# Performance work log

Measured on AMD Instinct MI355X. Metric: run time of the kernel, lower is better.

The kernel has to match this reference:

```python
import jax, jax.numpy as jnp
import numpy as np

N, E, IN_DIM, D, T, L, B, SLEN, C = 50000, 600000, 128, 128, 4, 2, 2048, 16, 16


def _deg_inv_sqrt(idx, n, dtype):
    deg = jax.ops.segment_sum(jnp.ones(idx.shape, dtype=dtype), idx, num_segments=n)
    return jnp.where(deg > 0, deg ** -0.5, 0.0).astype(dtype)


def gcn_conv(h, edge_index, W, b):
    # PyG GCNConv: add self loops, symmetric norm, x@W, scatter-add, +bias
    n = h.shape[0]
    loop = jnp.arange(n)
    row = jnp.concatenate([edge_index[0], loop])
    col = jnp.concatenate([edge_index[1], loop])
    dis = _deg_inv_sqrt(col, n, h.dtype)
    norm = dis[row] * dis[col]              # [E+N]
    xw = h @ W                               # [N, D]
    msgs = xw[row] * norm[:, None]           # [E+N, D] gather
    out = jax.ops.segment_sum(msgs, col, num_segments=n)
    return out + b


def re_conv(r, edge_index, node_type, W, wtype, b):
    # REConv(norm='both'): left-norm by src out-degree, x@W, type weight,
    # scatter-add to dst, right-norm by dst in-degree, +bias, relu
    n = r.shape[0]
    row, col = edge_index
    dl = _deg_inv_sqrt(row, n, r.dtype)
    x = (r * dl[:, None]) @ W                # [N, T]
    x = x * wtype[node_type][:, None]
    out = jax.ops.segment_sum(x[row], col, num_segments=n)
    dr = _deg_inv_sqrt(col, n, r.dtype)
    out = out * dr[:, None] + b
    return jax.nn.relu(out)


def setup_inputs() -> dict:
    key = jax.random.key(0)
    ks = jax.random.split(key, 10)
    x = jax.random.normal(ks[0], (N, IN_DIM), dtype=jnp.float32)
    label = jax.random.randint(ks[1], (N,), 0, C)
    seqs = jax.random.randint(ks[2], (B, SLEN), 0, N)
    edge_index = jax.random.randint(ks[3], (2, E), 0, N)
    node_type = jnp.sort(jax.random.randint(ks[4], (N,), 0, T))
    s_in = 1.0 / np.sqrt(IN_DIM)
    s_d = 1.0 / np.sqrt(D)
    fcW = jax.random.normal(ks[5], (T, IN_DIM, D), dtype=jnp.float32) * s_in
    fcB = jnp.zeros((T, D), dtype=jnp.float32)
    gcnW = jax.random.normal(ks[6], (L, D, D), dtype=jnp.float32) * s_d
    gcnB = jnp.zeros((L, D), dtype=jnp.float32)
    reW = jax.random.normal(ks[7], (L, T, T), dtype=jnp.float32) * 0.5
    re_wtype = jnp.ones((L, T), dtype=jnp.float32)
    reB = jnp.zeros((L, T), dtype=jnp.float32)
    predW = jax.random.normal(ks[8], (D, C), dtype=jnp.float32) * s_d
    predB = jnp.zeros((C,), dtype=jnp.float32)
    return {"x": x, "label": label, "seqs": seqs, "edge_index": edge_index,
            "node_type": node_type, "fcW": fcW, "fcB": fcB, "gcnW": gcnW,
            "gcnB": gcnB, "reW": reW, "re_wtype": re_wtype, "reB": reB,
            "predW": predW, "predB": predB}


def reference(x, label, seqs, edge_index, node_type, fcW, fcB, gcnW, gcnB,
              reW, re_wtype, reB, predW, predB):
    n = x.shape[0]
    # per-type input projection; node_type is sorted so this equals
    # torch.cat([fc[t](x[node_type==t]) for t])
    h_all = jnp.einsum('ni,tio->tno', x, fcW) + fcB[:, None, :]  # [T, N, D]
    gh = h_all[node_type, jnp.arange(n)]                          # [N, D]
    r = jnp.eye(fcW.shape[0], dtype=x.dtype)[node_type]           # [N, T]
    for l in range(gcnW.shape[0]):
        gh = jax.nn.relu(gcn_conv(gh, edge_index, gcnW[l], gcnB[l]))
        r = re_conv(r, edge_index, node_type, reW[l], re_wtype[l], reB[l])
    ego = seqs[:, 0]
    output = gh[ego] @ predW + predB                               # [B, C]
    return output, label[ego]
```

## Files before the change

kernel.cpp:

```cpp
#include <hip/hip_runtime.h>
#include <hip/hip_bf16.h>


typedef __attribute__((ext_vector_type(8))) short short8;
typedef __attribute__((ext_vector_type(4))) float f32x4;
typedef unsigned short u16;

__device__ __forceinline__ float bf2f(u16 u) {
  union { float f; unsigned int i; } v; v.i = (unsigned int)u << 16; return v.f;
}
__device__ __forceinline__ u16 f2bf(float f) {
  union { float f; unsigned int i; } v; v.f = f;
  return (u16)((v.i + 0x7FFF + ((v.i >> 16) & 1)) >> 16);
}

#define NPB 128

__global__ void k_wt(const float* __restrict__ fcW, const float* __restrict__ gcnW,
                     u16* __restrict__ wt, int T, int total) {
  int i = blockIdx.x * 256 + threadIdx.x;
  if (i >= total) return;
  int m = i >> 14;
  int dk = i & 16383;
  int d = dk >> 7, k = dk & 127;
  const float* src = (m < T) ? (fcW + ((size_t)m << 14)) : (gcnW + ((size_t)(m - T) << 14));
  wt[i] = f2bf(src[k * 128 + d]);
}

#define SWZ(row, byte) ((byte) ^ (((row) & 15) << 4))

__device__ __forceinline__ void stage_tile_bf16(char* smem, const u16* __restrict__ gsrc,
                                                int rows_valid, int t) {
  int row = t >> 1;
  int h = (t & 1) * 64;
  int byte0 = row * 256 + h * 2;
  if (row < rows_valid) {
    const u16* src = gsrc + (size_t)row * 128 + h;
#pragma unroll
    for (int j = 0; j < 8; ++j) {
      short8 v = *(const short8*)(src + j * 8);
      *(short8*)(smem + SWZ(row, byte0 + j * 16)) = v;
    }
  } else {
    short8 z = (short8){0, 0, 0, 0, 0, 0, 0, 0};
#pragma unroll
    for (int j = 0; j < 8; ++j)
      *(short8*)(smem + SWZ(row, byte0 + j * 16)) = z;
  }
}

__device__ __forceinline__ void mfma_core128(const char* xs, const char* wt, int t,
                                             f32x4 acc[8][2]) {
  const int lane = t & 63, w = t >> 6;
  const int lr = lane & 15, lk = lane >> 4;
  short8 bfrag[4][2];
#pragma unroll
  for (int ks = 0; ks < 4; ++ks) {
    int kb = ks * 64 + lk * 16;
#pragma unroll
    for (int ch = 0; ch < 2; ++ch) {
      int row = w * 32 + ch * 16 + lr;
      bfrag[ks][ch] = *(const short8*)(wt + SWZ(row, row * 256 + kb));
    }
  }
#pragma unroll
  for (int ks = 0; ks < 4; ++ks) {
    int kb = ks * 64 + lk * 16;
    short8 a[8];
#pragma unroll
    for (int rg = 0; rg < 8; ++rg) {
      int row = rg * 16 + lr;
      a[rg] = *(const short8*)(xs + SWZ(row, row * 256 + kb));
    }
#pragma unroll
    for (int rg = 0; rg < 8; ++rg)
#pragma unroll
      for (int ch = 0; ch < 2; ++ch)
        acc[rg][ch] = __builtin_amdgcn_mfma_f32_16x16x32_bf16(a[rg], bfrag[ks][ch],
                                                              acc[rg][ch], 0, 0, 0);
  }
}

__global__ __launch_bounds__(256) void k_fc(const float* __restrict__ x,
                                            const int* __restrict__ node_type,
                                            const u16* __restrict__ wt_fc,
                                            const float* __restrict__ fcB,
                                            u16* __restrict__ gh, int n_nodes) {
  __shared__ char smem[65536];
  char* smem_xs = smem;
  char* smem_wt = smem + 32768;
  const int t = threadIdx.x;
  const int nbase = blockIdx.x * NPB;
  const int nend = min(nbase + NPB, n_nodes);
  const int t0 = node_type[nbase];
  const int t1 = node_type[nend - 1];

  {
    int row = t >> 1;
    int h = (t & 1) * 64;
    int node = nbase + row;
    int byte0 = row * 256 + h * 2;
    if (node < n_nodes) {
      const float4* src = (const float4*)(x + (size_t)node * 128 + h);
#pragma unroll
      for (int j = 0; j < 8; ++j) {
        float4 a4 = src[j * 2], b4 = src[j * 2 + 1];
        u16 tmp[8] = {f2bf(a4.x), f2bf(a4.y), f2bf(a4.z), f2bf(a4.w),
                      f2bf(b4.x), f2bf(b4.y), f2bf(b4.z), f2bf(b4.w)};
        *(short8*)(smem_xs + SWZ(row, byte0 + j * 16)) = *(short8*)tmp;
      }
    } else {
      short8 z = (short8){0, 0, 0, 0, 0, 0, 0, 0};
#pragma unroll
      for (int j = 0; j < 8; ++j)
        *(short8*)(smem_xs + SWZ(row, byte0 + j * 16)) = z;
    }
  }

  const int lane = t & 63, w = t >> 6;
  const int lr = lane & 15, lk = lane >> 4;

  for (int tt = t0; tt <= t1; ++tt) {
    if (tt > t0) __syncthreads();
    stage_tile_bf16(smem_wt, wt_fc + ((size_t)tt << 14), 128, t);
    __syncthreads();

    f32x4 acc[8][2];
#pragma unroll
    for (int rg = 0; rg < 8; ++rg)
#pragma unroll
      for (int ch = 0; ch < 2; ++ch) acc[rg][ch] = (f32x4){0.f, 0.f, 0.f, 0.f};
    mfma_core128(smem_xs, smem_wt, t, acc);

    float bv0 = fcB[tt * 128 + w * 32 + lr];
    float bv1 = fcB[tt * 128 + w * 32 + 16 + lr];
#pragma unroll
    for (int rg = 0; rg < 8; ++rg) {
#pragma unroll
      for (int reg = 0; reg < 4; ++reg) {
        int node = nbase + rg * 16 + lk * 4 + reg;
        if (node < n_nodes && node_type[node] == tt) {
          gh[(size_t)node * 128 + w * 32 + lr]      = f2bf(acc[rg][0][reg] + bv0);
          gh[(size_t)node * 128 + w * 32 + 16 + lr] = f2bf(acc[rg][1][reg] + bv1);
        }
      }
    }
  }
}

__global__ __launch_bounds__(256) void k_gemm_scale(const u16* __restrict__ ghin,
                                                    const u16* __restrict__ wtg,
                                                    const float* __restrict__ dis,
                                                    u16* __restrict__ xws, int n_nodes) {
  __shared__ char smem[65536];
  char* smem_xs = smem;
  char* smem_wt = smem + 32768;
  const int t = threadIdx.x;
  const int nbase = blockIdx.x * NPB;

  stage_tile_bf16(smem_xs, ghin + (size_t)nbase * 128,
                  min(n_nodes - nbase, NPB), t);
  stage_tile_bf16(smem_wt, wtg, 128, t);
  __syncthreads();

  f32x4 acc[8][2];
#pragma unroll
  for (int rg = 0; rg < 8; ++rg)
#pragma unroll
    for (int ch = 0; ch < 2; ++ch) acc[rg][ch] = (f32x4){0.f, 0.f, 0.f, 0.f};
  mfma_core128(smem_xs, smem_wt, t, acc);

  const int lane = t & 63, w = t >> 6;
  const int lr = lane & 15, lk = lane >> 4;
#pragma unroll
  for (int rg = 0; rg < 8; ++rg) {
#pragma unroll
    for (int reg = 0; reg < 4; ++reg) {
      int node = nbase + rg * 16 + lk * 4 + reg;
      if (node < n_nodes) {
        float s = dis[node];
        xws[(size_t)node * 128 + w * 32 + lr]      = f2bf(acc[rg][0][reg] * s);
        xws[(size_t)node * 128 + w * 32 + 16 + lr] = f2bf(acc[rg][1][reg] * s);
      }
    }
  }
}

__global__ void k_zero(int* __restrict__ p, int n) {
  int i = blockIdx.x * 256 + threadIdx.x;
  if (i < n) p[i] = 0;
}

__global__ void k_count(const int* __restrict__ col, int* __restrict__ ecnt, int e) {
  int i = blockIdx.x * 256 + threadIdx.x;
  if (i < e) atomicAdd(&ecnt[col[i]], 1);
}

__global__ __launch_bounds__(256) void k_scan1(const int* __restrict__ ecnt,
                                               int* __restrict__ scanex,
                                               int* __restrict__ partials, int n) {
  __shared__ int s[256];
  const int t = threadIdx.x;
  const int i = blockIdx.x * 256 + t;
  int v = (i < n) ? ecnt[i] : 0;
  s[t] = v;
  __syncthreads();
  for (int off = 1; off < 256; off <<= 1) {
    int add = (t >= off) ? s[t - off] : 0;
    __syncthreads();
    s[t] += add;
    __syncthreads();
  }
  if (i < n) scanex[i] = s[t] - v;
  if (t == 255) partials[blockIdx.x] = s[t];
}

__global__ __launch_bounds__(256) void k_scan2(int* __restrict__ partials, int np) {
  __shared__ int s[256];
  const int t = threadIdx.x;
  int v = (t < np) ? partials[t] : 0;
  s[t] = v;
  __syncthreads();
  for (int off = 1; off < 256; off <<= 1) {
    int add = (t >= off) ? s[t - off] : 0;
    __syncthreads();
    s[t] += add;
    __syncthreads();
  }
  if (t < np) partials[t] = s[t] - v;
}

__global__ void k_scan3(const int* __restrict__ scanex, const int* __restrict__ partials,
                        const int* __restrict__ ecnt, int* __restrict__ col_ptr,
                        int* __restrict__ cursor, float* __restrict__ dis,
                        int n, int e_total) {
  int i = blockIdx.x * 256 + threadIdx.x;
  if (i < n) {
    int p = scanex[i] + partials[i >> 8];
    col_ptr[i] = p;
    cursor[i] = p;
    dis[i] = rsqrtf((float)(ecnt[i] + 1));
  }
  if (i == 0) col_ptr[n] = e_total;
}

__global__ void k_fill(const int* __restrict__ row, const int* __restrict__ col,
                       int* __restrict__ cursor, int* __restrict__ edge_row, int e) {
  int i = blockIdx.x * 256 + threadIdx.x;
  if (i < e) {
    int c = col[i];
    int pos = atomicAdd(&cursor[c], 1);
    edge_row[pos] = row[i];
  }
}

__device__ __forceinline__ void gather_node(int node, const int* __restrict__ col_ptr,
                                            const int* __restrict__ edge_row,
                                            const u16* __restrict__ xws,
                                            const float* __restrict__ dis,
                                            const float* __restrict__ bias,
                                            u16* __restrict__ dst, int lane) {
  const int g = lane & 15;
  const int s = lane >> 4;
  float acc[8] = {0.f, 0.f, 0.f, 0.f, 0.f, 0.f, 0.f, 0.f};
  if (s == 0) {
    short8 v = *(const short8*)(xws + (size_t)node * 128 + g * 8);
#pragma unroll
    for (int j = 0; j < 8; ++j) acc[j] = bf2f((u16)v[j]);
  }
  const int e0 = col_ptr[node], e1 = col_ptr[node + 1];
  for (int e = e0 + s; e < e1; e += 4) {
    int r = edge_row[e];
    short8 v = *(const short8*)(xws + (size_t)r * 128 + g * 8);
#pragma unroll
    for (int j = 0; j < 8; ++j) acc[j] += bf2f((u16)v[j]);
  }
#pragma unroll
  for (int j = 0; j < 8; ++j) {
    acc[j] += __shfl_xor(acc[j], 16);
    acc[j] += __shfl_xor(acc[j], 32);
  }
  if (s == 0) {
    float ds = dis[node];
    u16 o[8];
#pragma unroll
    for (int j = 0; j < 8; ++j)
      o[j] = f2bf(fmaxf(acc[j] * ds + bias[g * 8 + j], 0.f));
    *(short8*)(dst + g * 8) = *(short8*)o;
  }
}

__global__ __launch_bounds__(256) void k_gather(const int* __restrict__ col_ptr,
                                                const int* __restrict__ edge_row,
                                                const u16* __restrict__ xws,
                                                const float* __restrict__ dis,
                                                const float* __restrict__ bias,
                                                u16* __restrict__ gh, int n_nodes) {
  const int t = threadIdx.x;
  const int node = blockIdx.x * 4 + (t >> 6);
  if (node >= n_nodes) return;
  gather_node(node, col_ptr, edge_row, xws, dis, bias,
              gh + (size_t)node * 128, t & 63);
}

__global__ __launch_bounds__(256) void k_gather_ego(const int* __restrict__ col_ptr,
                                                    const int* __restrict__ edge_row,
                                                    const u16* __restrict__ xws,
                                                    const float* __restrict__ dis,
                                                    const float* __restrict__ bias,
                                                    const int* __restrict__ seqs,
                                                    u16* __restrict__ gh2,
                                                    int b_total, int slen) {
  const int t = threadIdx.x;
  const int b = blockIdx.x * 4 + (t >> 6);
  if (b >= b_total) return;
  int node = seqs[(size_t)b * slen];
  gather_node(node, col_ptr, edge_row, xws, dis, bias,
              gh2 + (size_t)b * 128, t & 63);
}

__global__ void k_pred(const u16* __restrict__ gh2, const int* __restrict__ seqs,
                       const int* __restrict__ label, const float* __restrict__ predW,
                       const float* __restrict__ predB, float* __restrict__ out,
                       float* __restrict__ out_label, int b_total, int n_classes,
                       int slen) {
  int tid = blockIdx.x * 256 + threadIdx.x;
  int b = tid / n_classes;
  if (b >= b_total) return;
  int c = tid - b * n_classes;
  const u16* g = gh2 + (size_t)b * 128;
  float s = predB[c];
#pragma unroll 8
  for (int i = 0; i < 128; ++i) s += bf2f(g[i]) * predW[i * n_classes + c];
  out[(size_t)b * n_classes + c] = s;
  if (c == 0) out_label[b] = (float)label[seqs[(size_t)b * slen]];
}

extern "C" void kernel_launch(void* const* d_in, const int* in_sizes, int n_in,
                              void* d_out, int out_size, void* d_ws, size_t ws_size,
                              hipStream_t stream) {
  const float* x     = (const float*)d_in[0];
  const int*   label = (const int*)d_in[1];
  const int*   seqs  = (const int*)d_in[2];
  const int*   edge  = (const int*)d_in[3];
  const int*   ntype = (const int*)d_in[4];
  const float* fcW   = (const float*)d_in[5];
  const float* fcB   = (const float*)d_in[6];
  const float* gcnW  = (const float*)d_in[7];
  const float* gcnB  = (const float*)d_in[8];
  const float* predW = (const float*)d_in[12];
  const float* predB = (const float*)d_in[13];

  const int n = in_sizes[0] / 128;
  const int e = in_sizes[3] / 2;
  const int T = in_sizes[5] / (128 * 128);
  const int L = in_sizes[8] / 128;
  const int C = in_sizes[13];
  const int slen = 16;
  const int b_total = in_sizes[2] / slen;

  const int* row = edge;
  const int* col = edge + e;

  char* ws = (char*)d_ws;
  const size_t node_bf = (size_t)n * 128 * sizeof(u16);
  u16*   gh      = (u16*)ws;                 ws += node_bf;
  u16*   xws     = (u16*)ws;                 ws += node_bf;
  u16*   gh2     = (u16*)ws;                 ws += (size_t)b_total * 128 * 2;
  u16*   wt      = (u16*)ws;                 ws += (size_t)(T + L) * 16384 * 2;
  float* dis     = (float*)ws;               ws += (size_t)n * 4;
  int*   ecnt    = (int*)ws;                 ws += (size_t)n * 4;
  int*   scanex  = (int*)ws;                 ws += (size_t)n * 4;
  int*   col_ptr = (int*)ws;                 ws += (size_t)(n + 16) * 4;
  int*   cursor  = (int*)ws;                 ws += (size_t)n * 4;
  int*   partial = (int*)ws;                 ws += 1024 * 4;
  int*   edge_row= (int*)ws;                 ws += (size_t)e * 4;

  float* out_logits = (float*)d_out;
  float* out_label  = out_logits + (size_t)b_total * C;

  const int nb = (n + NPB - 1) / NPB;
  const int nscan = (n + 255) / 256;
  const int wt_total = (T + L) * 16384;

  hipLaunchKernelGGL(k_wt, dim3((wt_total + 255) / 256), dim3(256), 0, stream,
                     fcW, gcnW, wt, T, wt_total);
  hipLaunchKernelGGL(k_fc, dim3(nb), dim3(256), 0, stream, x, ntype, wt, fcB, gh, n);

  hipLaunchKernelGGL(k_zero, dim3(nscan), dim3(256), 0, stream, ecnt, n);
  hipLaunchKernelGGL(k_count, dim3((e + 255) / 256), dim3(256), 0, stream, col, ecnt, e);
  hipLaunchKernelGGL(k_scan1, dim3(nscan), dim3(256), 0, stream, ecnt, scanex, partial, n);
  hipLaunchKernelGGL(k_scan2, dim3(1), dim3(256), 0, stream, partial, nscan);
  hipLaunchKernelGGL(k_scan3, dim3(nscan), dim3(256), 0, stream, scanex, partial, ecnt,
                     col_ptr, cursor, dis, n, e);
  hipLaunchKernelGGL(k_fill, dim3((e + 255) / 256), dim3(256), 0, stream, row, col,
                     cursor, edge_row, e);

  for (int l = 0; l < L; ++l) {
    hipLaunchKernelGGL(k_gemm_scale, dim3(nb), dim3(256), 0, stream,
                       gh, wt + (size_t)(T + l) * 16384, dis, xws, n);
    if (l < L - 1) {
      hipLaunchKernelGGL(k_gather, dim3((n + 3) / 4), dim3(256), 0, stream,
                         col_ptr, edge_row, xws, dis, gcnB + (size_t)l * 128, gh, n);
    } else {
      hipLaunchKernelGGL(k_gather_ego, dim3((b_total + 3) / 4), dim3(256), 0, stream,
                         col_ptr, edge_row, xws, dis, gcnB + (size_t)l * 128,
                         seqs, gh2, b_total, slen);
    }
  }
  hipLaunchKernelGGL(k_pred, dim3((b_total * C + 255) / 256), dim3(256), 0, stream,
                     gh2, seqs, label, predW, predB, out_logits, out_label,
                     b_total, C, slen);
}
```

Before: 259.9 us.

## Fuse all stages into one cooperative persistent kernel with grid syncs

Replaces about twelve separate kernel launches with one cooperative megakernel. Stages are separated by grid.sync, and independent work is overlapped within a stage: the edge counting runs alongside the fc projection, and the CSR fill runs alongside the first GEMM. This removes launch overhead and inter-kernel gaps. The cost is a grid limited to at most 512 resident blocks looping over tiles, lower occupancy from launch bounds of 2 blocks per CU with 64KB of shared memory, and several grid-wide barriers, each of which has a cost.

After: 837.4 us. +222.2%, slower.

```diff
diff --git a/kernel.cpp b/kernel.cpp
--- a/kernel.cpp
+++ b/kernel.cpp
@@ -1,5 +1,8 @@
 #include <hip/hip_runtime.h>
 #include <hip/hip_bf16.h>
+#include <hip/hip_cooperative_groups.h>
+
+namespace cg = cooperative_groups;
 
 
 typedef __attribute__((ext_vector_type(8))) short short8;
@@ -15,21 +18,21 @@
 }
 
 #define NPB 128
-
-__global__ void k_wt(const float* __restrict__ fcW, const float* __restrict__ gcnW,
-                     u16* __restrict__ wt, int T, int total) {
-  int i = blockIdx.x * 256 + threadIdx.x;
-  if (i >= total) return;
-  int m = i >> 14;
-  int dk = i & 16383;
-  int d = dk >> 7, k = dk & 127;
-  const float* src = (m < T) ? (fcW + ((size_t)m << 14)) : (gcnW + ((size_t)(m - T) << 14));
-  wt[i] = f2bf(src[k * 128 + d]);
-}
-
 #define SWZ(row, byte) ((byte) ^ (((row) & 15) << 4))
 
-__device__ __forceinline__ void stage_tile_bf16(char* smem, const u16* __restrict__ gsrc,
+struct MegaParams {
+  const float* x; const int* label; const int* seqs;
+  const int* row; const int* col; const int* ntype;
+  const float* fcW; const float* fcB; const float* gcnW; const float* gcnB;
+  const float* predW; const float* predB;
+  u16* gh; u16* xws; u16* gh2; u16* wt;
+  float* dis; int* ecnt; int* scanex; int* col_ptr; int* cursor; int* partial;
+  int* edge_row;
+  float* out_logits; float* out_label;
+  int n, e, T, L, C, slen, b_total;
+};
+
+__device__ __forceinline__ void stage_tile_bf16(char* smem, const u16* gsrc,
                                                 int rows_valid, int t) {
   int row = t >> 1;
   int h = (t & 1) * 64;
@@ -81,39 +84,34 @@
   }
 }
 
-__global__ __launch_bounds__(256) void k_fc(const float* __restrict__ x,
-                                            const int* __restrict__ node_type,
-                                            const u16* __restrict__ wt_fc,
-                                            const float* __restrict__ fcB,
-                                            u16* __restrict__ gh, int n_nodes) {
-  __shared__ char smem[65536];
-  char* smem_xs = smem;
-  char* smem_wt = smem + 32768;
-  const int t = threadIdx.x;
-  const int nbase = blockIdx.x * NPB;
-  const int nend = min(nbase + NPB, n_nodes);
-  const int t0 = node_type[nbase];
-  const int t1 = node_type[nend - 1];
+__device__ void fc_tile(const MegaParams& p, int tile, int t, char* smem) {
+  __syncthreads();
+  char* xs = smem;
+  char* wtl = smem + 32768;
+  const int nbase = tile * NPB;
+  const int nend = min(nbase + NPB, p.n);
+  const int t0 = p.ntype[nbase];
+  const int t1 = p.ntype[nend - 1];
 
   {
     int row = t >> 1;
     int h = (t & 1) * 64;
     int node = nbase + row;
     int byte0 = row * 256 + h * 2;
-    if (node < n_nodes) {
-      const float4* src = (const float4*)(x + (size_t)node * 128 + h);
+    if (node < p.n) {
+      const float4* src = (const float4*)(p.x + (size_t)node * 128 + h);
 #pragma unroll
       for (int j = 0; j < 8; ++j) {
         float4 a4 = src[j * 2], b4 = src[j * 2 + 1];
         u16 tmp[8] = {f2bf(a4.x), f2bf(a4.y), f2bf(a4.z), f2bf(a4.w),
                       f2bf(b4.x), f2bf(b4.y), f2bf(b4.z), f2bf(b4.w)};
-        *(short8*)(smem_xs + SWZ(row, byte0 + j * 16)) = *(short8*)tmp;
+        *(short8*)(xs + SWZ(row, byte0 + j * 16)) = *(short8*)tmp;
       }
     } else {
       short8 z = (short8){0, 0, 0, 0, 0, 0, 0, 0};
 #pragma unroll
       for (int j = 0; j < 8; ++j)
-        *(short8*)(smem_xs + SWZ(row, byte0 + j * 16)) = z;
+        *(short8*)(xs + SWZ(row, byte0 + j * 16)) = z;
     }
   }
 
@@ -121,54 +119,49 @@
   const int lr = lane & 15, lk = lane >> 4;
 
   for (int tt = t0; tt <= t1; ++tt) {
-    if (tt > t0) __syncthreads();
-    stage_tile_bf16(smem_wt, wt_fc + ((size_t)tt << 14), 128, t);
     __syncthreads();
+    stage_tile_bf16(wtl, p.wt + ((size_t)tt << 14), 128, t);
+    __syncthreads();
 
     f32x4 acc[8][2];
 #pragma unroll
     for (int rg = 0; rg < 8; ++rg)
 #pragma unroll
       for (int ch = 0; ch < 2; ++ch) acc[rg][ch] = (f32x4){0.f, 0.f, 0.f, 0.f};
-    mfma_core128(smem_xs, smem_wt, t, acc);
-
-    float bv0 = fcB[tt * 128 + w * 32 + lr];
-    float bv1 = fcB[tt * 128 + w * 32 + 16 + lr];
+    mfma_core128(xs, wtl, t, acc);
+
+    float bv0 = p.fcB[tt * 128 + w * 32 + lr];
+    float bv1 = p.fcB[tt * 128 + w * 32 + 16 + lr];
 #pragma unroll
     for (int rg = 0; rg < 8; ++rg) {
 #pragma unroll
       for (int reg = 0; reg < 4; ++reg) {
         int node = nbase + rg * 16 + lk * 4 + reg;
-        if (node < n_nodes && node_type[node] == tt) {
-          gh[(size_t)node * 128 + w * 32 + lr]      = f2bf(acc[rg][0][reg] + bv0);
-          gh[(size_t)node * 128 + w * 32 + 16 + lr] = f2bf(acc[rg][1][reg] + bv1);
+        if (node < p.n && p.ntype[node] == tt) {
+          p.gh[(size_t)node * 128 + w * 32 + lr]      = f2bf(acc[rg][0][reg] + bv0);
+          p.gh[(size_t)node * 128 + w * 32 + 16 + lr] = f2bf(acc[rg][1][reg] + bv1);
         }
       }
     }
   }
 }
 
-__global__ __launch_bounds__(256) void k_gemm_scale(const u16* __restrict__ ghin,
-                                                    const u16* __restrict__ wtg,
-                                                    const float* __restrict__ dis,
-                                                    u16* __restrict__ xws, int n_nodes) {
-  __shared__ char smem[65536];
-  char* smem_xs = smem;
-  char* smem_wt = smem + 32768;
-  const int t = threadIdx.x;
-  const int nbase = blockIdx.x * NPB;
-
-  stage_tile_bf16(smem_xs, ghin + (size_t)nbase * 128,
-                  min(n_nodes - nbase, NPB), t);
-  stage_tile_bf16(smem_wt, wtg, 128, t);
+__device__ void gemm_tile(const MegaParams& p, const u16* wtg, int tile, int t,
+                          char* smem) {
   __syncthreads();
+  char* xs = smem;
+  char* wtl = smem + 32768;
+  const int nbase = tile * NPB;
+  stage_tile_bf16(xs, p.gh + (size_t)nbase * 128, min(p.n - nbase, NPB), t);
+  stage_tile_bf16(wtl, wtg, 128, t);
+  __syncthreads();
 
   f32x4 acc[8][2];
 #pragma unroll
   for (int rg = 0; rg < 8; ++rg)
 #pragma unroll
     for (int ch = 0; ch < 2; ++ch) acc[rg][ch] = (f32x4){0.f, 0.f, 0.f, 0.f};
-  mfma_core128(smem_xs, smem_wt, t, acc);
+  mfma_core128(xs, wtl, t, acc);
 
   const int lane = t & 63, w = t >> 6;
   const int lr = lane & 15, lk = lane >> 4;
@@ -177,89 +170,19 @@
 #pragma unroll
     for (int reg = 0; reg < 4; ++reg) {
       int node = nbase + rg * 16 + lk * 4 + reg;
-      if (node < n_nodes) {
-        float s = dis[node];
-        xws[(size_t)node * 128 + w * 32 + lr]      = f2bf(acc[rg][0][reg] * s);
-        xws[(size_t)node * 128 + w * 32 + 16 + lr] = f2bf(acc[rg][1][reg] * s);
-      }
-    }
-  }
-}
-
-__global__ void k_zero(int* __restrict__ p, int n) {
-  int i = blockIdx.x * 256 + threadIdx.x;
-  if (i < n) p[i] = 0;
-}
-
-__global__ void k_count(const int* __restrict__ col, int* __restrict__ ecnt, int e) {
-  int i = blockIdx.x * 256 + threadIdx.x;
-  if (i < e) atomicAdd(&ecnt[col[i]], 1);
-}
-
-__global__ __launch_bounds__(256) void k_scan1(const int* __restrict__ ecnt,
-                                               int* __restrict__ scanex,
-                                               int* __restrict__ partials, int n) {
-  __shared__ int s[256];
-  const int t = threadIdx.x;
-  const int i = blockIdx.x * 256 + t;
-  int v = (i < n) ? ecnt[i] : 0;
-  s[t] = v;
-  __syncthreads();
-  for (int off = 1; off < 256; off <<= 1) {
-    int add = (t >= off) ? s[t - off] : 0;
-    __syncthreads();
-    s[t] += add;
-    __syncthreads();
-  }
-  if (i < n) scanex[i] = s[t] - v;
-  if (t == 255) partials[blockIdx.x] = s[t];
-}
-
-__global__ __launch_bounds__(256) void k_scan2(int* __restrict__ partials, int np) {
-  __shared__ int s[256];
-  const int t = threadIdx.x;
-  int v = (t < np) ? partials[t] : 0;
-  s[t] = v;
-  __syncthreads();
-  for (int off = 1; off < 256; off <<= 1) {
-    int add = (t >= off) ? s[t - off] : 0;
-    __syncthreads();
-    s[t] += add;
-    __syncthreads();
-  }
-  if (t < np) partials[t] = s[t] - v;
-}
-
-__global__ void k_scan3(const int* __restrict__ scanex, const int* __restrict__ partials,
-                        const int* __restrict__ ecnt, int* __restrict__ col_ptr,
-                        int* __restrict__ cursor, float* __restrict__ dis,
-                        int n, int e_total) {
-  int i = blockIdx.x * 256 + threadIdx.x;
-  if (i < n) {
-    int p = scanex[i] + partials[i >> 8];
-    col_ptr[i] = p;
-    cursor[i] = p;
-    dis[i] = rsqrtf((float)(ecnt[i] + 1));
-  }
-  if (i == 0) col_ptr[n] = e_total;
-}
-
-__global__ void k_fill(const int* __restrict__ row, const int* __restrict__ col,
-                       int* __restrict__ cursor, int* __restrict__ edge_row, int e) {
-  int i = blockIdx.x * 256 + threadIdx.x;
-  if (i < e) {
-    int c = col[i];
-    int pos = atomicAdd(&cursor[c], 1);
-    edge_row[pos] = row[i];
-  }
-}
-
-__device__ __forceinline__ void gather_node(int node, const int* __restrict__ col_ptr,
-                                            const int* __restrict__ edge_row,
-                                            const u16* __restrict__ xws,
-                                            const float* __restrict__ dis,
-                                            const float* __restrict__ bias,
-                                            u16* __restrict__ dst, int lane) {
+      if (node < p.n) {
+        float s = p.dis[node];
+        p.xws[(size_t)node * 128 + w * 32 + lr]      = f2bf(acc[rg][0][reg] * s);
+        p.xws[(size_t)node * 128 + w * 32 + 16 + lr] = f2bf(acc[rg][1][reg] * s);
+      }
+    }
+  }
+}
+
+__device__ __forceinline__ void gather_node(int node, const int* col_ptr,
+                                            const int* edge_row, const u16* xws,
+                                            const float* dis, const float* bias,
+                                            u16* dst, int lane) {
   const int g = lane & 15;
   const int s = lane >> 4;
   float acc[8] = {0.f, 0.f, 0.f, 0.f, 0.f, 0.f, 0.f, 0.f};
@@ -290,67 +213,120 @@
   }
 }
 
-__global__ __launch_bounds__(256) void k_gather(const int* __restrict__ col_ptr,
-                                                const int* __restrict__ edge_row,
-                                                const u16* __restrict__ xws,
-                                                const float* __restrict__ dis,
-                                                const float* __restrict__ bias,
-                                                u16* __restrict__ gh, int n_nodes) {
+__global__ __launch_bounds__(256, 2) void k_mega(MegaParams p) {
+  __shared__ char smem[65536];
+  cg::grid_group grid = cg::this_grid();
   const int t = threadIdx.x;
-  const int node = blockIdx.x * 4 + (t >> 6);
-  if (node >= n_nodes) return;
-  gather_node(node, col_ptr, edge_row, xws, dis, bias,
-              gh + (size_t)node * 128, t & 63);
-}
-
-__global__ __launch_bounds__(256) void k_gather_ego(const int* __restrict__ col_ptr,
-                                                    const int* __restrict__ edge_row,
-                                                    const u16* __restrict__ xws,
-                                                    const float* __restrict__ dis,
-                                                    const float* __restrict__ bias,
-                                                    const int* __restrict__ seqs,
-                                                    u16* __restrict__ gh2,
-                                                    int b_total, int slen) {
-  const int t = threadIdx.x;
-  const int b = blockIdx.x * 4 + (t >> 6);
-  if (b >= b_total) return;
-  int node = seqs[(size_t)b * slen];
-  gather_node(node, col_ptr, edge_row, xws, dis, bias,
-              gh2 + (size_t)b * 128, t & 63);
-}
-
-__global__ void k_pred(const u16* __restrict__ gh2, const int* __restrict__ seqs,
-                       const int* __restrict__ label, const float* __restrict__ predW,
-                       const float* __restrict__ predB, float* __restrict__ out,
-                       float* __restrict__ out_label, int b_total, int n_classes,
-                       int slen) {
-  int tid = blockIdx.x * 256 + threadIdx.x;
-  int b = tid / n_classes;
-  if (b >= b_total) return;
-  int c = tid - b * n_classes;
-  const u16* g = gh2 + (size_t)b * 128;
-  float s = predB[c];
+  const int b = blockIdx.x;
+  const int G = gridDim.x;
+  const int gt = b * 256 + t;
+  const int GT = G * 256;
+  const int nb = (p.n + NPB - 1) / NPB;
+  const int nscan = (p.n + 255) / 256;
+
+  {
+    const int wt_total = (p.T + p.L) * 16384;
+    for (int i = gt; i < wt_total; i += GT) {
+      int m = i >> 14, dk = i & 16383, d = dk >> 7, k = dk & 127;
+      const float* src = (m < p.T) ? (p.fcW + ((size_t)m << 14))
+                                   : (p.gcnW + ((size_t)(m - p.T) << 14));
+      p.wt[i] = f2bf(src[k * 128 + d]);
+    }
+    for (int i = gt; i < p.n; i += GT) p.ecnt[i] = 0;
+  }
+  __threadfence(); grid.sync();
+
+  for (int tile = b; tile < nb; tile += G) fc_tile(p, tile, t, smem);
+  for (int i = gt; i < p.e; i += GT) atomicAdd(&p.ecnt[p.col[i]], 1);
+  __threadfence(); grid.sync();
+
+  for (int chunk = b; chunk < nscan; chunk += G) {
+    __syncthreads();
+    int* s = (int*)smem;
+    int i = chunk * 256 + t;
+    int v = (i < p.n) ? p.ecnt[i] : 0;
+    s[t] = v; __syncthreads();
+    for (int off = 1; off < 256; off <<= 1) {
+      int add = (t >= off) ? s[t - off] : 0; __syncthreads();
+      s[t] += add; __syncthreads();
+    }
+    if (i < p.n) p.scanex[i] = s[t] - v;
+    if (t == 255) p.partial[chunk] = s[t];
+  }
+  __threadfence(); grid.sync();
+
+  if (b == 0) {
+    __syncthreads();
+    int* s = (int*)smem;
+    int v = (t < nscan) ? p.partial[t] : 0;
+    s[t] = v; __syncthreads();
+    for (int off = 1; off < 256; off <<= 1) {
+      int add = (t >= off) ? s[t - off] : 0; __syncthreads();
+      s[t] += add; __syncthreads();
+    }
+    if (t < nscan) p.partial[t] = s[t] - v;
+  }
+  __threadfence(); grid.sync();
+
+  for (int i = gt; i < p.n; i += GT) {
+    int pos = p.scanex[i] + p.partial[i >> 8];
+    p.col_ptr[i] = pos;
+    p.cursor[i] = pos;
+    p.dis[i] = rsqrtf((float)(p.ecnt[i] + 1));
+  }
+  if (gt == 0) p.col_ptr[p.n] = p.e;
+  __threadfence(); grid.sync();
+
+  for (int l = 0; l < p.L; ++l) {
+    const u16* wl = p.wt + (size_t)(p.T + l) * 16384;
+    for (int tile = b; tile < nb; tile += G) gemm_tile(p, wl, tile, t, smem);
+    if (l == 0) {
+      for (int i = gt; i < p.e; i += GT) {
+        int c = p.col[i];
+        int pos = atomicAdd(&p.cursor[c], 1);
+        p.edge_row[pos] = p.row[i];
+      }
+    }
+    __threadfence(); grid.sync();
+
+    const float* bias = p.gcnB + (size_t)l * 128;
+    const int lane = t & 63;
+    if (l < p.L - 1) {
+      const int ngrp = (p.n + 3) / 4;
+      for (int grp = b; grp < ngrp; grp += G) {
+        int node = grp * 4 + (t >> 6);
+        if (node < p.n)
+          gather_node(node, p.col_ptr, p.edge_row, p.xws, p.dis, bias,
+                      p.gh + (size_t)node * 128, lane);
+      }
+    } else {
+      const int ngrp = (p.b_total + 3) / 4;
+      for (int grp = b; grp < ngrp; grp += G) {
+        int bb = grp * 4 + (t >> 6);
+        if (bb < p.b_total) {
+          int node = p.seqs[(size_t)bb * p.slen];
+          gather_node(node, p.col_ptr, p.edge_row, p.xws, p.dis, bias,
+                      p.gh2 + (size_t)bb * 128, lane);
+        }
+      }
+    }
+    __threadfence(); grid.sync();
+  }
+
+  for (int i = gt; i < p.b_total * p.C; i += GT) {
+    int bb = i / p.C, c = i - bb * p.C;
+    const u16* g = p.gh2 + (size_t)bb * 128;
+    float s = p.predB[c];
 #pragma unroll 8
-  for (int i = 0; i < 128; ++i) s += bf2f(g[i]) * predW[i * n_classes + c];
-  out[(size_t)b * n_classes + c] = s;
-  if (c == 0) out_label[b] = (float)label[seqs[(size_t)b * slen]];
+    for (int k = 0; k < 128; ++k) s += bf2f(g[k]) * p.predW[k * p.C + c];
+    p.out_logits[i] = s;
+    if (c == 0) p.out_label[bb] = (float)p.label[p.seqs[(size_t)bb * p.slen]];
+  }
 }
 
 extern "C" void kernel_launch(void* const* d_in, const int* in_sizes, int n_in,
                               void* d_out, int out_size, void* d_ws, size_t ws_size,
                               hipStream_t stream) {
-  const float* x     = (const float*)d_in[0];
-  const int*   label = (const int*)d_in[1];
-  const int*   seqs  = (const int*)d_in[2];
-  const int*   edge  = (const int*)d_in[3];
-  const int*   ntype = (const int*)d_in[4];
-  const float* fcW   = (const float*)d_in[5];
-  const float* fcB   = (const float*)d_in[6];
-  const float* gcnW  = (const float*)d_in[7];
-  const float* gcnB  = (const float*)d_in[8];
-  const float* predW = (const float*)d_in[12];
-  const float* predB = (const float*)d_in[13];
-
   const int n = in_sizes[0] / 128;
   const int e = in_sizes[3] / 2;
   const int T = in_sizes[5] / (128 * 128);
@@ -359,56 +335,51 @@
   const int slen = 16;
   const int b_total = in_sizes[2] / slen;
 
-  const int* row = edge;
-  const int* col = edge + e;
-
   char* ws = (char*)d_ws;
   const size_t node_bf = (size_t)n * 128 * sizeof(u16);
-  u16*   gh      = (u16*)ws;                 ws += node_bf;
-  u16*   xws     = (u16*)ws;                 ws += node_bf;
-  u16*   gh2     = (u16*)ws;                 ws += (size_t)b_total * 128 * 2;
-  u16*   wt      = (u16*)ws;                 ws += (size_t)(T + L) * 16384 * 2;
-  float* dis     = (float*)ws;               ws += (size_t)n * 4;
-  int*   ecnt    = (int*)ws;                 ws += (size_t)n * 4;
-  int*   scanex  = (int*)ws;                 ws += (size_t)n * 4;
-  int*   col_ptr = (int*)ws;                 ws += (size_t)(n + 16) * 4;
-  int*   cursor  = (int*)ws;                 ws += (size_t)n * 4;
-  int*   partial = (int*)ws;                 ws += 1024 * 4;
-  int*   edge_row= (int*)ws;                 ws += (size_t)e * 4;
-
-  float* out_logits = (float*)d_out;
-  float* out_label  = out_logits + (size_t)b_total * C;
-
-  const int nb = (n + NPB - 1) / NPB;
-  const int nscan = (n + 255) / 256;
-  const int wt_total = (T + L) * 16384;
-
-  hipLaunchKernelGGL(k_wt, dim3((wt_total + 255) / 256), dim3(256), 0, stream,
-                     fcW, gcnW, wt, T, wt_total);
-  hipLaunchKernelGGL(k_fc, dim3(nb), dim3(256), 0, stream, x, ntype, wt, fcB, gh, n);
-
-  hipLaunchKernelGGL(k_zero, dim3(nscan), dim3(256), 0, stream, ecnt, n);
-  hipLaunchKernelGGL(k_count, dim3((e + 255) / 256), dim3(256), 0, stream, col, ecnt, e);
-  hipLaunchKernelGGL(k_scan1, dim3(nscan), dim3(256), 0, stream, ecnt, scanex, partial, n);
-  hipLaunchKernelGGL(k_scan2, dim3(1), dim3(256), 0, stream, partial, nscan);
-  hipLaunchKernelGGL(k_scan3, dim3(nscan), dim3(256), 0, stream, scanex, partial, ecnt,
-                     col_ptr, cursor, dis, n, e);
-  hipLaunchKernelGGL(k_fill, dim3((e + 255) / 256), dim3(256), 0, stream, row, col,
-                     cursor, edge_row, e);
-
-  for (int l = 0; l < L; ++l) {
-    hipLaunchKernelGGL(k_gemm_scale, dim3(nb), dim3(256), 0, stream,
-                       gh, wt + (size_t)(T + l) * 16384, dis, xws, n);
-    if (l < L - 1) {
-      hipLaunchKernelGGL(k_gather, dim3((n + 3) / 4), dim3(256), 0, stream,
-                         col_ptr, edge_row, xws, dis, gcnB + (size_t)l * 128, gh, n);
-    } else {
-      hipLaunchKernelGGL(k_gather_ego, dim3((b_total + 3) / 4), dim3(256), 0, stream,
-                         col_ptr, edge_row, xws, dis, gcnB + (size_t)l * 128,
-                         seqs, gh2, b_total, slen);
-    }
-  }
-  hipLaunchKernelGGL(k_pred, dim3((b_total * C + 255) / 256), dim3(256), 0, stream,
-                     gh2, seqs, label, predW, predB, out_logits, out_label,
-                     b_total, C, slen);
-}
+
+  MegaParams p;
+  p.x     = (const float*)d_in[0];
+  p.label = (const int*)d_in[1];
+  p.seqs  = (const int*)d_in[2];
+  p.row   = (const int*)d_in[3];
+  p.col   = ((const int*)d_in[3]) + e;
+  p.ntype = (const int*)d_in[4];
+  p.fcW   = (const float*)d_in[5];
+  p.fcB   = (const float*)d_in[6];
+  p.gcnW  = (const float*)d_in[7];
+  p.gcnB  = (const float*)d_in[8];
+  p.predW = (const float*)d_in[12];
+  p.predB = (const float*)d_in[13];
+
+  p.gh      = (u16*)ws;                 ws += node_bf;
+  p.xws     = (u16*)ws;                 ws += node_bf;
+  p.gh2     = (u16*)ws;                 ws += (size_t)b_total * 128 * 2;
+  p.wt      = (u16*)ws;                 ws += (size_t)(T + L) * 16384 * 2;
+  p.dis     = (float*)ws;               ws += (size_t)n * 4;
+  p.ecnt    = (int*)ws;                 ws += (size_t)n * 4;
+  p.scanex  = (int*)ws;                 ws += (size_t)n * 4;
+  p.col_ptr = (int*)ws;                 ws += (size_t)(n + 16) * 4;
+  p.cursor  = (int*)ws;                 ws += (size_t)n * 4;
+  p.partial = (int*)ws;                 ws += 1024 * 4;
+  p.edge_row= (int*)ws;                 ws += (size_t)e * 4;
+
+  p.out_logits = (float*)d_out;
+  p.out_label  = p.out_logits + (size_t)b_total * C;
+
+  p.n = n; p.e = e; p.T = T; p.L = L; p.C = C; p.slen = slen; p.b_total = b_total;
+
+  int dev = 0;
+  hipGetDevice(&dev);
+  int mp = 0;
+  hipDeviceGetAttribute(&mp, hipDeviceAttributeMultiprocessorCount, dev);
+  if (mp <= 0) mp = 256;
+  int perCU = 0;
+  hipOccupancyMaxActiveBlocksPerMultiprocessor(&perCU, k_mega, 256, 0);
+  if (perCU < 1) perCU = 1;
+  long cap = (long)mp * perCU;
+  int G = (int)(cap < 512 ? cap : 512);
+
+  void* args[] = { &p };
+  hipLaunchCooperativeKernel((void*)k_mega, dim3(G), dim3(256), args, 0, stream);
+}
```

## Fuse prep, degree counting, CSR fill and prediction into neighboring kernels

Applied to the files above, without the earlier changes.

Folds the weight transpose and counter zeroing into one grid-stride prep kernel. It also moves the edge degree count into the tail of the fc GEMM kernel and the CSR fill into the first gcn GEMM kernel. The ego gather and the prediction matmul are merged into one kernel that keeps the gathered row in shared memory. This removes several launches and their serialization gaps, but it ties the atomic-heavy edge passes to GEMM blocks, which may lengthen those kernels.

Result: faster. 248.6 us (-4.4%).

```diff
diff --git a/kernel.cpp b/kernel.cpp
--- a/kernel.cpp
+++ b/kernel.cpp
@@ -15,19 +15,20 @@
 }
 
 #define NPB 128
-
-__global__ void k_wt(const float* __restrict__ fcW, const float* __restrict__ gcnW,
-                     u16* __restrict__ wt, int T, int total) {
-  int i = blockIdx.x * 256 + threadIdx.x;
-  if (i >= total) return;
-  int m = i >> 14;
-  int dk = i & 16383;
-  int d = dk >> 7, k = dk & 127;
-  const float* src = (m < T) ? (fcW + ((size_t)m << 14)) : (gcnW + ((size_t)(m - T) << 14));
-  wt[i] = f2bf(src[k * 128 + d]);
-}
-
 #define SWZ(row, byte) ((byte) ^ (((row) & 15) << 4))
+
+__global__ void k_prep(const float* __restrict__ fcW, const float* __restrict__ gcnW,
+                       u16* __restrict__ wt, int* __restrict__ ecnt,
+                       int T, int wt_total, int n) {
+  const int gt = blockIdx.x * 256 + threadIdx.x;
+  const int GT = gridDim.x * 256;
+  for (int i = gt; i < wt_total; i += GT) {
+    int m = i >> 14, dk = i & 16383, d = dk >> 7, k = dk & 127;
+    const float* src = (m < T) ? (fcW + ((size_t)m << 14)) : (gcnW + ((size_t)(m - T) << 14));
+    wt[i] = f2bf(src[k * 128 + d]);
+  }
+  for (int i = gt; i < n; i += GT) ecnt[i] = 0;
+}
 
 __device__ __forceinline__ void stage_tile_bf16(char* smem, const u16* __restrict__ gsrc,
                                                 int rows_valid, int t) {
@@ -85,7 +86,9 @@
                                             const int* __restrict__ node_type,
                                             const u16* __restrict__ wt_fc,
                                             const float* __restrict__ fcB,
-                                            u16* __restrict__ gh, int n_nodes) {
+                                            u16* __restrict__ gh, int n_nodes,
+                                            const int* __restrict__ col,
+                                            int* __restrict__ ecnt, int e_edges) {
   __shared__ char smem[65536];
   char* smem_xs = smem;
   char* smem_wt = smem + 32768;
@@ -146,20 +149,28 @@
       }
     }
   }
+
+  const int gt = blockIdx.x * 256 + t;
+  const int GT = gridDim.x * 256;
+  for (int i = gt; i < e_edges; i += GT) atomicAdd(&ecnt[col[i]], 1);
 }
 
 __global__ __launch_bounds__(256) void k_gemm_scale(const u16* __restrict__ ghin,
                                                     const u16* __restrict__ wtg,
                                                     const float* __restrict__ dis,
-                                                    u16* __restrict__ xws, int n_nodes) {
+                                                    u16* __restrict__ xws, int n_nodes,
+                                                    const int* __restrict__ row,
+                                                    const int* __restrict__ col,
+                                                    int* __restrict__ cursor,
+                                                    int* __restrict__ edge_row,
+                                                    int e_edges, int do_fill) {
   __shared__ char smem[65536];
   char* smem_xs = smem;
   char* smem_wt = smem + 32768;
   const int t = threadIdx.x;
   const int nbase = blockIdx.x * NPB;
 
-  stage_tile_bf16(smem_xs, ghin + (size_t)nbase * 128,
-                  min(n_nodes - nbase, NPB), t);
+  stage_tile_bf16(smem_xs, ghin + (size_t)nbase * 128, min(n_nodes - nbase, NPB), t);
   stage_tile_bf16(smem_wt, wtg, 128, t);
   __syncthreads();
 
@@ -184,16 +195,16 @@
       }
     }
   }
-}
-
-__global__ void k_zero(int* __restrict__ p, int n) {
-  int i = blockIdx.x * 256 + threadIdx.x;
-  if (i < n) p[i] = 0;
-}
-
-__global__ void k_count(const int* __restrict__ col, int* __restrict__ ecnt, int e) {
-  int i = blockIdx.x * 256 + threadIdx.x;
-  if (i < e) atomicAdd(&ecnt[col[i]], 1);
+
+  if (do_fill) {
+    const int gt = blockIdx.x * 256 + t;
+    const int GT = gridDim.x * 256;
+    for (int i = gt; i < e_edges; i += GT) {
+      int c = col[i];
+      int pos = atomicAdd(&cursor[c], 1);
+      edge_row[pos] = row[i];
+    }
+  }
 }
 
 __global__ __launch_bounds__(256) void k_scan1(const int* __restrict__ ecnt,
@@ -242,16 +253,6 @@
     dis[i] = rsqrtf((float)(ecnt[i] + 1));
   }
   if (i == 0) col_ptr[n] = e_total;
-}
-
-__global__ void k_fill(const int* __restrict__ row, const int* __restrict__ col,
-                       int* __restrict__ cursor, int* __restrict__ edge_row, int e) {
-  int i = blockIdx.x * 256 + threadIdx.x;
-  if (i < e) {
-    int c = col[i];
-    int pos = atomicAdd(&cursor[c], 1);
-    edge_row[pos] = row[i];
-  }
 }
 
 __device__ __forceinline__ void gather_node(int node, const int* __restrict__ col_ptr,
@@ -303,37 +304,40 @@
               gh + (size_t)node * 128, t & 63);
 }
 
-__global__ __launch_bounds__(256) void k_gather_ego(const int* __restrict__ col_ptr,
-                                                    const int* __restrict__ edge_row,
-                                                    const u16* __restrict__ xws,
-                                                    const float* __restrict__ dis,
-                                                    const float* __restrict__ bias,
-                                                    const int* __restrict__ seqs,
-                                                    u16* __restrict__ gh2,
-                                                    int b_total, int slen) {
-  const int t = threadIdx.x;
-  const int b = blockIdx.x * 4 + (t >> 6);
-  if (b >= b_total) return;
-  int node = seqs[(size_t)b * slen];
-  gather_node(node, col_ptr, edge_row, xws, dis, bias,
-              gh2 + (size_t)b * 128, t & 63);
-}
-
-__global__ void k_pred(const u16* __restrict__ gh2, const int* __restrict__ seqs,
-                       const int* __restrict__ label, const float* __restrict__ predW,
-                       const float* __restrict__ predB, float* __restrict__ out,
-                       float* __restrict__ out_label, int b_total, int n_classes,
-                       int slen) {
-  int tid = blockIdx.x * 256 + threadIdx.x;
-  int b = tid / n_classes;
-  if (b >= b_total) return;
-  int c = tid - b * n_classes;
-  const u16* g = gh2 + (size_t)b * 128;
-  float s = predB[c];
+__global__ __launch_bounds__(256) void k_egopred(const int* __restrict__ col_ptr,
+                                                 const int* __restrict__ edge_row,
+                                                 const u16* __restrict__ xws,
+                                                 const float* __restrict__ dis,
+                                                 const float* __restrict__ bias,
+                                                 const int* __restrict__ seqs,
+                                                 const int* __restrict__ label,
+                                                 const float* __restrict__ predW,
+                                                 const float* __restrict__ predB,
+                                                 float* __restrict__ out,
+                                                 float* __restrict__ out_label,
+                                                 int b_total, int n_classes, int slen) {
+  __shared__ u16 buf[4][128];
+  const int t = threadIdx.x;
+  const int w = t >> 6, lane = t & 63;
+  const int b = blockIdx.x * 4 + w;
+  int node = -1;
+  if (b < b_total) {
+    node = seqs[(size_t)b * slen];
+    gather_node(node, col_ptr, edge_row, xws, dis, bias, &buf[w][0], lane);
+  }
+  __syncthreads();
+  if (b < b_total) {
+    const int c = lane & 15;
+    const int q = lane >> 4;
+    float s = 0.f;
 #pragma unroll 8
-  for (int i = 0; i < 128; ++i) s += bf2f(g[i]) * predW[i * n_classes + c];
-  out[(size_t)b * n_classes + c] = s;
-  if (c == 0) out_label[b] = (float)label[seqs[(size_t)b * slen]];
+    for (int k = q * 32; k < q * 32 + 32; ++k)
+      s += bf2f(buf[w][k]) * predW[k * n_classes + c];
+    s += __shfl_xor(s, 16);
+    s += __shfl_xor(s, 32);
+    if (q == 0) out[(size_t)b * n_classes + c] = s + predB[c];
+    if (lane == 0) out_label[b] = (float)label[node];
+  }
 }
 
 extern "C" void kernel_launch(void* const* d_in, const int* in_sizes, int n_in,
@@ -366,7 +370,6 @@
   const size_t node_bf = (size_t)n * 128 * sizeof(u16);
   u16*   gh      = (u16*)ws;                 ws += node_bf;
   u16*   xws     = (u16*)ws;                 ws += node_bf;
-  u16*   gh2     = (u16*)ws;                 ws += (size_t)b_total * 128 * 2;
   u16*   wt      = (u16*)ws;                 ws += (size_t)(T + L) * 16384 * 2;
   float* dis     = (float*)ws;               ws += (size_t)n * 4;
   int*   ecnt    = (int*)ws;                 ws += (size_t)n * 4;
@@ -383,32 +386,27 @@
   const int nscan = (n + 255) / 256;
   const int wt_total = (T + L) * 16384;
 
-  hipLaunchKernelGGL(k_wt, dim3((wt_total + 255) / 256), dim3(256), 0, stream,
-                     fcW, gcnW, wt, T, wt_total);
-  hipLaunchKernelGGL(k_fc, dim3(nb), dim3(256), 0, stream, x, ntype, wt, fcB, gh, n);
-
-  hipLaunchKernelGGL(k_zero, dim3(nscan), dim3(256), 0, stream, ecnt, n);
-  hipLaunchKernelGGL(k_count, dim3((e + 255) / 256), dim3(256), 0, stream, col, ecnt, e);
+  hipLaunchKernelGGL(k_prep, dim3(384), dim3(256), 0, stream,
+                     fcW, gcnW, wt, ecnt, T, wt_total, n);
+  hipLaunchKernelGGL(k_fc, dim3(nb), dim3(256), 0, stream,
+                     x, ntype, wt, fcB, gh, n, col, ecnt, e);
   hipLaunchKernelGGL(k_scan1, dim3(nscan), dim3(256), 0, stream, ecnt, scanex, partial, n);
   hipLaunchKernelGGL(k_scan2, dim3(1), dim3(256), 0, stream, partial, nscan);
   hipLaunchKernelGGL(k_scan3, dim3(nscan), dim3(256), 0, stream, scanex, partial, ecnt,
                      col_ptr, cursor, dis, n, e);
-  hipLaunchKernelGGL(k_fill, dim3((e + 255) / 256), dim3(256), 0, stream, row, col,
-                     cursor, edge_row, e);
 
   for (int l = 0; l < L; ++l) {
     hipLaunchKernelGGL(k_gemm_scale, dim3(nb), dim3(256), 0, stream,
-                       gh, wt + (size_t)(T + l) * 16384, dis, xws, n);
+                       gh, wt + (size_t)(T + l) * 16384, dis, xws, n,
+                       row, col, cursor, edge_row, e, (l == 0) ? 1 : 0);
     if (l < L - 1) {
       hipLaunchKernelGGL(k_gather, dim3((n + 3) / 4), dim3(256), 0, stream,
                          col_ptr, edge_row, xws, dis, gcnB + (size_t)l * 128, gh, n);
     } else {
-      hipLaunchKernelGGL(k_gather_ego, dim3((b_total + 3) / 4), dim3(256), 0, stream,
+      hipLaunchKernelGGL(k_egopred, dim3((b_total + 3) / 4), dim3(256), 0, stream,
                          col_ptr, edge_row, xws, dis, gcnB + (size_t)l * 128,
-                         seqs, gh2, b_total, slen);
-    }
-  }
-  hipLaunchKernelGGL(k_pred, dim3((b_total * C + 255) / 256), dim3(256), 0, stream,
-                     gh2, seqs, label, predW, predB, out_logits, out_label,
-                     b_total, C, slen);
-}
+                         seqs, label, predW, predB, out_logits, out_label,
+                         b_total, C, slen);
+    }
+  }
+}
```
